# Performance work log

Measured on AMD Instinct MI355X. Metric: run time of the kernel, lower is better.

Reference implementation:

```python
import jax, jax.numpy as jnp
import numpy as np

D_MODEL = 1024
N_HEADS = 16
D_K = D_MODEL // N_HEADS
B, S = 2, 2048
NEG = -1.0e9


def setup_inputs() -> dict:
    key = jax.random.key(0)
    ks = jax.random.split(key, 12)
    sc = 1.0 / np.sqrt(D_MODEL)
    inp = {
        'query': jax.random.normal(ks[0], (B, S, D_MODEL), jnp.float32),
        'key': jax.random.normal(ks[1], (B, S, D_MODEL), jnp.float32),
        'value': jax.random.normal(ks[2], (B, S, D_MODEL), jnp.float32),
        # causal mask, broadcast over batch: 1 = attend, 0 = masked
        'mask': jnp.broadcast_to(jnp.tril(jnp.ones((S, S), jnp.int32)), (B, S, S)),
        'wq': jax.random.normal(ks[3], (D_MODEL, D_MODEL), jnp.float32) * sc,
        'bq': jnp.zeros((D_MODEL,), jnp.float32),
        'wk': jax.random.normal(ks[4], (D_MODEL, D_MODEL), jnp.float32) * sc,
        'bk': jnp.zeros((D_MODEL,), jnp.float32),
        'wv': jax.random.normal(ks[5], (D_MODEL, D_MODEL), jnp.float32) * sc,
        'bv': jnp.zeros((D_MODEL,), jnp.float32),
        'wo': jax.random.normal(ks[6], (D_MODEL, D_MODEL), jnp.float32) * sc,
        'bo': jnp.zeros((D_MODEL,), jnp.float32),
    }
    return inp


def reference(query, key, value, mask, wq, bq, wk, bk, wv, bv, wo, bo):
    b, sq, _ = query.shape
    sk = key.shape[1]
    # linear projections, split into heads: [B, H, S, d_k]
    def proj(x, w, bias, s):
        return (x @ w + bias).reshape(b, s, N_HEADS, D_K).transpose(0, 2, 1, 3)
    Q = proj(query, wq, bq, sq)
    K = proj(key, wk, bk, sk)
    V = proj(value, wv, bv, sk)
    # scaled dot-product attention with full score matrix [B, H, Sq, Sk]
    scores = jnp.einsum('bhqd,bhkd->bhqk', Q, K) / np.sqrt(D_K)
    scores = jnp.where(mask[:, None, :, :] == 0, NEG, scores)
    attn = jax.nn.softmax(scores, axis=-1)
    ctx = jnp.einsum('bhqk,bhkd->bhqd', attn, V)
    ctx = ctx.transpose(0, 2, 1, 3).reshape(b, sq, D_MODEL)
    return ctx @ wo + bo
```

## Files before the change

kernel.cpp:

```cpp
#include <hip/hip_runtime.h>
#include <stdint.h>

#define AS1 __attribute__((address_space(1)))
#define AS3 __attribute__((address_space(3)))

typedef __attribute__((ext_vector_type(8))) __bf16 bf16x8;
typedef __attribute__((ext_vector_type(4))) float f32x4;
typedef __attribute__((ext_vector_type(4))) unsigned int u32x4;
typedef __attribute__((ext_vector_type(2))) unsigned int u32x2;

static __device__ __forceinline__ void gload16(const void* g, void* l) {
    __builtin_amdgcn_global_load_lds((AS1 void*)(uintptr_t)g, (AS3 void*)l, 16, 0, 0);
}

static __device__ __forceinline__ unsigned cvt_pk_bf16(float lo, float hi) {
    unsigned r;
    asm volatile("v_cvt_pk_bf16_f32 %0, %1, %2" : "=v"(r) : "v"(lo), "v"(hi));
    return r;
}
static __device__ __forceinline__ unsigned short f2bf(float f) {
    return (unsigned short)(cvt_pk_bf16(f, 0.f) & 0xffffu);
}

static __device__ __forceinline__ f32x4 mfma16(bf16x8 a, bf16x8 b, f32x4 c) {
    return __builtin_amdgcn_mfma_f32_16x16x32_bf16(a, b, c, 0, 0, 0);
}

static __device__ __forceinline__ float fexp2(float x) {
    return __builtin_amdgcn_exp2f(x);
}

__global__ __launch_bounds__(256) void k_wtrans4(const float* __restrict__ w0,
                                                 const float* __restrict__ w1,
                                                 const float* __restrict__ w2,
                                                 const float* __restrict__ w3,
                                                 unsigned short* __restrict__ o0,
                                                 unsigned short* __restrict__ o1,
                                                 unsigned short* __restrict__ o2,
                                                 unsigned short* __restrict__ o3) {
    const float* W;
    unsigned short* Wt;
    switch (blockIdx.z) {
        case 0: W = w0; Wt = o0; break;
        case 1: W = w1; Wt = o1; break;
        case 2: W = w2; Wt = o2; break;
        default: W = w3; Wt = o3; break;
    }
    __shared__ unsigned short tile[64][72];
    const int tid = threadIdx.x;
    const int k0 = blockIdx.x * 64, n0 = blockIdx.y * 64;
#pragma unroll
    for (int j = 0; j < 4; ++j) {
        int c = j * 256 + tid;
        int kr = c >> 4, c4 = c & 15;
        f32x4 v = *(const f32x4*)(W + (size_t)(k0 + kr) * 1024 + n0 + c4 * 4);
#pragma unroll
        for (int e = 0; e < 4; ++e) tile[c4 * 4 + e][kr] = f2bf(v[e]);
    }
    __syncthreads();
#pragma unroll
    for (int j = 0; j < 2; ++j) {
        int c = j * 256 + tid;
        int nr = c >> 3, kc = c & 7;
        union { unsigned short s[8]; u32x4 v; } t;
#pragma unroll
        for (int e = 0; e < 8; ++e) t.s[e] = tile[nr][kc * 8 + e];
        *(u32x4*)(Wt + (size_t)(n0 + nr) * 1024 + k0 + kc * 8) = t.v;
    }
}

__global__ __launch_bounds__(256) void k_cvt3(const float* __restrict__ q,
                                              const float* __restrict__ k,
                                              const float* __restrict__ v,
                                              unsigned short* __restrict__ oq,
                                              unsigned short* __restrict__ ok,
                                              unsigned short* __restrict__ ov) {
    const float* src; unsigned short* dst;
    switch (blockIdx.z) {
        case 0: src = q; dst = oq; break;
        case 1: src = k; dst = ok; break;
        default: src = v; dst = ov; break;
    }
    const size_t i = ((size_t)blockIdx.x * 256 + threadIdx.x) * 8;
    f32x4 a = *(const f32x4*)(src + i);
    f32x4 b = *(const f32x4*)(src + i + 4);
    u32x4 o;
    o[0] = cvt_pk_bf16(a[0], a[1]);
    o[1] = cvt_pk_bf16(a[2], a[3]);
    o[2] = cvt_pk_bf16(b[0], b[1]);
    o[3] = cvt_pk_bf16(b[2], b[3]);
    *(u32x4*)(dst + i) = o;
}

template <int A_F32, int OUT_F32>
static __device__ __forceinline__ void gemm_body(const void* __restrict__ Ap,
                                                 const unsigned short* __restrict__ Bt,
                                                 const float* __restrict__ bias,
                                                 void* __restrict__ Cp,
                                                 int M, int N, int K, float cscale,
                                                 char* smem) {
    constexpr int ASZ = A_F32 ? 16384 : 8192;
    char* sA = smem;
    char* sB = smem + 2 * ASZ;
    const int tid = threadIdx.x;
    const int wave = tid >> 6, lane = tid & 63, g = lane >> 4, l16 = lane & 15;
    const int wm = wave & 1, wn = wave >> 1;
    const int m0 = blockIdx.x * 64, n0 = blockIdx.y * 128;

    f32x4 acc[2][4];
#pragma unroll
    for (int i = 0; i < 2; ++i)
#pragma unroll
        for (int j = 0; j < 4; ++j) acc[i][j] = (f32x4){0.f, 0.f, 0.f, 0.f};

    auto STAGE = [&](int k0, int buf) {
        if constexpr (A_F32) {
            const float* A = (const float*)Ap;
            char* dst = sA + buf * ASZ;
#pragma unroll
            for (int j = 0; j < 4; ++j) {
                int c = j * 256 + tid;
                int row = c >> 4, w = c & 15, kc = w ^ (row & 15);
                gload16(A + (size_t)(m0 + row) * K + k0 + kc * 4, dst + c * 16);
            }
        } else {
            const unsigned short* A = (const unsigned short*)Ap;
            char* dst = sA + buf * ASZ;
#pragma unroll
            for (int j = 0; j < 2; ++j) {
                int c = j * 256 + tid;
                int row = c >> 3, w = c & 7, kc = w ^ (row & 7);
                gload16(A + (size_t)(m0 + row) * K + k0 + kc * 8, dst + c * 16);
            }
        }
        char* dst = sB + buf * 16384;
#pragma unroll
        for (int j = 0; j < 4; ++j) {
            int c = j * 256 + tid;
            int row = c >> 3, w = c & 7, kc = w ^ (row & 7);
            gload16(Bt + (size_t)(n0 + row) * K + k0 + kc * 8, dst + c * 16);
        }
    };

    const int nkt = K >> 6;
    STAGE(0, 0);
    __syncthreads();
    int cur = 0;
#pragma unroll 1
    for (int kt = 0; kt < nkt; ++kt) {
        if (kt + 1 < nkt) STAGE((kt + 1) << 6, cur ^ 1);
        const char* sAc = sA + cur * ASZ;
        const char* sBc = sB + cur * 16384;
#pragma unroll
        for (int ks = 0; ks < 2; ++ks) {
            bf16x8 af[2];
#pragma unroll
            for (int mi = 0; mi < 2; ++mi) {
                int row = wm * 32 + mi * 16 + l16;
                if constexpr (A_F32) {
                    int c0 = (ks * 8 + g * 2) ^ (row & 15);
                    int c1 = (ks * 8 + g * 2 + 1) ^ (row & 15);
                    f32x4 lo = *(const f32x4*)(sAc + row * 256 + c0 * 16);
                    f32x4 hi = *(const f32x4*)(sAc + row * 256 + c1 * 16);
                    union { unsigned u[4]; bf16x8 v; } cv;
                    cv.u[0] = cvt_pk_bf16(lo[0], lo[1]);
                    cv.u[1] = cvt_pk_bf16(lo[2], lo[3]);
                    cv.u[2] = cvt_pk_bf16(hi[0], hi[1]);
                    cv.u[3] = cvt_pk_bf16(hi[2], hi[3]);
                    af[mi] = cv.v;
                } else {
                    int c = (ks * 4 + g) ^ (row & 7);
                    af[mi] = *(const bf16x8*)(sAc + row * 128 + c * 16);
                }
            }
#pragma unroll
            for (int ni = 0; ni < 4; ++ni) {
                int row = wn * 64 + ni * 16 + l16;
                int c = (ks * 4 + g) ^ (row & 7);
                bf16x8 bfr = *(const bf16x8*)(sBc + row * 128 + c * 16);
#pragma unroll
                for (int mi = 0; mi < 2; ++mi)
                    acc[mi][ni] = mfma16(af[mi], bfr, acc[mi][ni]);
            }
        }
        __syncthreads();
        cur ^= 1;
    }
#pragma unroll
    for (int ni = 0; ni < 4; ++ni) {
        int col = n0 + wn * 64 + ni * 16 + l16;
        float bn = bias[col];
#pragma unroll
        for (int mi = 0; mi < 2; ++mi) {
            int rbase = m0 + wm * 32 + mi * 16 + g * 4;
#pragma unroll
            for (int r = 0; r < 4; ++r) {
                float v = (acc[mi][ni][r] + bn) * cscale;
                if constexpr (OUT_F32)
                    ((float*)Cp)[(size_t)(rbase + r) * N + col] = v;
                else
                    ((unsigned short*)Cp)[(size_t)(rbase + r) * N + col] = f2bf(v);
            }
        }
    }
}

__global__ __launch_bounds__(256) void k_gemm_qkv(
    const unsigned short* __restrict__ Aq, const unsigned short* __restrict__ Ak,
    const unsigned short* __restrict__ Av,
    const unsigned short* __restrict__ Wq, const unsigned short* __restrict__ Wk,
    const unsigned short* __restrict__ Wv,
    const float* __restrict__ bq, const float* __restrict__ bk, const float* __restrict__ bv,
    unsigned short* __restrict__ Q2, unsigned short* __restrict__ K2,
    unsigned short* __restrict__ V2) {
    extern __shared__ __align__(16) char smem[];
    const unsigned short* A; const unsigned short* Bt; const float* bias;
    unsigned short* C; float sc;
    switch (blockIdx.z) {
        case 0:  A = Aq; Bt = Wq; bias = bq; C = Q2; sc = 0.18033688011112042f; break;
        case 1:  A = Ak; Bt = Wk; bias = bk; C = K2; sc = 1.0f; break;
        default: A = Av; Bt = Wv; bias = bv; C = V2; sc = 1.0f; break;
    }
    gemm_body<0, 0>(A, Bt, bias, C, 4096, 1024, 1024, sc, smem);
}

__global__ __launch_bounds__(256) void k_gemm_o(const unsigned short* __restrict__ ctx,
                                                const unsigned short* __restrict__ Wo,
                                                const float* __restrict__ bo,
                                                float* __restrict__ out) {
    extern __shared__ __align__(16) char smem[];
    gemm_body<0, 1>(ctx, Wo, bo, out, 4096, 1024, 1024, 1.0f, smem);
}

__global__ __launch_bounds__(256) void k_vtrans(const unsigned short* __restrict__ V2,
                                                unsigned short* __restrict__ Vt) {
    __shared__ unsigned short tile[64][72];
    const int tid = threadIdx.x;
    const int s0 = blockIdx.x * 64;
    const int bh = blockIdx.y, b = bh >> 4, h = bh & 15;
#pragma unroll
    for (int j = 0; j < 2; ++j) {
        int c = j * 256 + tid;
        int sr = c >> 3, dc = c & 7;
        union { u32x4 v; unsigned short s[8]; } t;
        t.v = *(const u32x4*)(V2 + (size_t)(b * 2048 + s0 + sr) * 1024 + h * 64 + dc * 8);
#pragma unroll
        for (int e = 0; e < 8; ++e) tile[dc * 8 + e][sr] = t.s[e];
    }
    __syncthreads();
#pragma unroll
    for (int j = 0; j < 2; ++j) {
        int c = j * 256 + tid;
        int dr = c >> 3, sc = c & 7;
        union { unsigned short s[8]; u32x4 v; } t;
#pragma unroll
        for (int e = 0; e < 8; ++e) t.s[e] = tile[dr][sc * 8 + e];
        *(u32x4*)(Vt + ((size_t)bh * 64 + dr) * 2048 + s0 + sc * 8) = t.v;
    }
}

__global__ __launch_bounds__(128) void k_attn(const unsigned short* __restrict__ Q2,
                                              const unsigned short* __restrict__ K2,
                                              const unsigned short* __restrict__ Vt,
                                              unsigned short* __restrict__ ctx) {
    __shared__ __align__(16) char sK[8192];
    __shared__ __align__(16) char sV[2][8192];
    __shared__ __align__(16) char sP[2][2][2048];

    const int tid = threadIdx.x, w = tid >> 6, lane = tid & 63;
    const int g = lane >> 4, l16 = lane & 15;
    const int bid = blockIdx.x;
    const int xcd = bid & 7, j = bid >> 3;
    const int bh = xcd * 4 + (j & 3);
    const int t = 31 - (j >> 2);
    const int b = bh >> 4, h = bh & 15;
    const int swzl = (l16 & 7) << 4;

    const int r0 = tid >> 3;
    const int sc0 = (tid & 7) ^ (r0 & 7);
    const unsigned short* ksrc = K2 + (size_t)(b * 2048 + r0) * 1024 + h * 64 + sc0 * 8;
    const unsigned short* vsrc = Vt + ((size_t)bh * 64 + r0) * 2048 + sc0 * 8;
    char* const myp0 = sP[w][0] + l16 * 128;
    char* const myp1 = sP[w][1] + l16 * 128;

    const int wq0 = t * 64 + w * 32;
    const int qg0 = wq0 + l16, qg1 = wq0 + 16 + l16;

    const unsigned short* qp0 = Q2 + (size_t)(b * 2048 + wq0 + l16) * 1024 + h * 64;
    const unsigned short* qp1 = qp0 + 16 * 1024;
    bf16x8 qf00 = *(const bf16x8*)(qp0 + g * 8);
    bf16x8 qf01 = *(const bf16x8*)(qp0 + 32 + g * 8);
    bf16x8 qf10 = *(const bf16x8*)(qp1 + g * 8);
    bf16x8 qf11 = *(const bf16x8*)(qp1 + 32 + g * 8);

    f32x4 accO0[4], accO1[4];
#pragma unroll
    for (int i = 0; i < 4; ++i) {
        accO0[i] = (f32x4){0.f, 0.f, 0.f, 0.f};
        accO1[i] = (f32x4){0.f, 0.f, 0.f, 0.f};
    }
    float m0 = 0.f, m1 = 0.f, lsum0 = 0.f, lsum1 = 0.f;

    const int nkv = t + 1;
#pragma unroll
    for (int rr = 0; rr < 4; ++rr) {
        gload16(ksrc + (size_t)(rr * 16) * 1024, sK + rr * 2048 + tid * 16);
        gload16(vsrc + (size_t)(rr * 16) * 2048, sV[0] + rr * 2048 + tid * 16);
    }
    __syncthreads();

    const unsigned short* kstage = ksrc + 64 * 1024;
    const unsigned short* vstage = vsrc + 64;

#pragma unroll 1
    for (int kt = 0; kt < nkv; ++kt) {
        const int cur = kt & 1;
        const int kv0 = kt * 64;
        float s0[16], s1[16];
        __builtin_amdgcn_s_setprio(1);
#pragma unroll
        for (int blk = 0; blk < 4; ++blk) {
            const int rl = blk * 16 + l16;
            const char* krow = sK + rl * 128;
            bf16x8 kf0 = *(const bf16x8*)(krow + ((g << 4) ^ swzl));
            bf16x8 kf1 = *(const bf16x8*)(krow + (((4 + g) << 4) ^ swzl));
            f32x4 a0 = (f32x4){0.f, 0.f, 0.f, 0.f};
            a0 = mfma16(kf0, qf00, a0);
            a0 = mfma16(kf1, qf01, a0);
            f32x4 a1 = (f32x4){0.f, 0.f, 0.f, 0.f};
            a1 = mfma16(kf0, qf10, a1);
            a1 = mfma16(kf1, qf11, a1);
#pragma unroll
            for (int rr = 0; rr < 4; ++rr) {
                s0[blk * 4 + rr] = a0[rr];
                s1[blk * 4 + rr] = a1[rr];
            }
        }
        __builtin_amdgcn_s_setprio(0);
        __syncthreads();
        if (kt + 1 < nkv) {
#pragma unroll
            for (int rr = 0; rr < 4; ++rr) {
                gload16(kstage + (size_t)(rr * 16) * 1024, sK + rr * 2048 + tid * 16);
                gload16(vstage + (size_t)(rr * 16) * 2048, sV[cur ^ 1] + rr * 2048 + tid * 16);
            }
            kstage += 64 * 1024;
            vstage += 64;
        }
        if (kt == t) {
#pragma unroll
            for (int j2 = 0; j2 < 16; ++j2) {
                int kvg = kv0 + (j2 >> 2) * 16 + g * 4 + (j2 & 3);
                if (kvg > qg0) s0[j2] = -1e9f;
                if (kvg > qg1) s1[j2] = -1e9f;
            }
        }
        float pa0 = 0.f, pa1 = 0.f, pa2 = 0.f, pa3 = 0.f;
        float pb0 = 0.f, pb1 = 0.f, pb2 = 0.f, pb3 = 0.f;
        unsigned pk0[8], pk1[8];
#pragma unroll
        for (int j2 = 0; j2 < 4; ++j2) {
            float a0 = fexp2(s0[4 * j2] - m0);
            float a1 = fexp2(s0[4 * j2 + 1] - m0);
            float a2 = fexp2(s0[4 * j2 + 2] - m0);
            float a3 = fexp2(s0[4 * j2 + 3] - m0);
            pa0 += a0; pa1 += a1; pa2 += a2; pa3 += a3;
            pk0[2 * j2] = cvt_pk_bf16(a0, a1);
            pk0[2 * j2 + 1] = cvt_pk_bf16(a2, a3);
            float b0 = fexp2(s1[4 * j2] - m1);
            float b1 = fexp2(s1[4 * j2 + 1] - m1);
            float b2 = fexp2(s1[4 * j2 + 2] - m1);
            float b3 = fexp2(s1[4 * j2 + 3] - m1);
            pb0 += b0; pb1 += b1; pb2 += b2; pb3 += b3;
            pk1[2 * j2] = cvt_pk_bf16(b0, b1);
            pk1[2 * j2 + 1] = cvt_pk_bf16(b2, b3);
        }
        float ps0 = (pa0 + pa1) + (pa2 + pa3);
        float ps1 = (pb0 + pb1) + (pb2 + pb3);
        if (__any(fmaxf(ps0, ps1) > 16777216.f)) {
            {
                float c1 = fmaxf(fmaxf(s0[0], s0[1]), fmaxf(s0[2], s0[3]));
                c1 = fmaxf(c1, fmaxf(fmaxf(s0[4], s0[5]), fmaxf(s0[6], s0[7])));
                float c2 = fmaxf(fmaxf(s0[8], s0[9]), fmaxf(s0[10], s0[11]));
                c2 = fmaxf(c2, fmaxf(fmaxf(s0[12], s0[13]), fmaxf(s0[14], s0[15])));
                float mx = fmaxf(c1, c2);
                mx = fmaxf(mx, __shfl_xor(mx, 16));
                mx = fmaxf(mx, __shfl_xor(mx, 32));
                float mnew = fmaxf(m0, mx);
                float scl = fexp2(m0 - mnew);
                lsum0 *= scl;
#pragma unroll
                for (int dt = 0; dt < 4; ++dt) accO0[dt] = accO0[dt] * scl;
                m0 = mnew;
                ps0 = 0.f;
#pragma unroll
                for (int j2 = 0; j2 < 8; ++j2) {
                    float p0 = fexp2(s0[2 * j2] - m0);
                    float p1 = fexp2(s0[2 * j2 + 1] - m0);
                    ps0 += p0 + p1;
                    pk0[j2] = cvt_pk_bf16(p0, p1);
                }
            }
            {
                float c1 = fmaxf(fmaxf(s1[0], s1[1]), fmaxf(s1[2], s1[3]));
                c1 = fmaxf(c1, fmaxf(fmaxf(s1[4], s1[5]), fmaxf(s1[6], s1[7])));
                float c2 = fmaxf(fmaxf(s1[8], s1[9]), fmaxf(s1[10], s1[11]));
                c2 = fmaxf(c2, fmaxf(fmaxf(s1[12], s1[13]), fmaxf(s1[14], s1[15])));
                float mx = fmaxf(c1, c2);
                mx = fmaxf(mx, __shfl_xor(mx, 16));
                mx = fmaxf(mx, __shfl_xor(mx, 32));
                float mnew = fmaxf(m1, mx);
                float scl = fexp2(m1 - mnew);
                lsum1 *= scl;
#pragma unroll
                for (int dt = 0; dt < 4; ++dt) accO1[dt] = accO1[dt] * scl;
                m1 = mnew;
                ps1 = 0.f;
#pragma unroll
                for (int j2 = 0; j2 < 8; ++j2) {
                    float p0 = fexp2(s1[2 * j2] - m1);
                    float p1 = fexp2(s1[2 * j2 + 1] - m1);
                    ps1 += p0 + p1;
                    pk1[j2] = cvt_pk_bf16(p0, p1);
                }
            }
        }
        lsum0 += ps0;
        lsum1 += ps1;
#pragma unroll
        for (int blk = 0; blk < 4; ++blk) {
            u32x2 pw0 = {pk0[blk * 2], pk0[blk * 2 + 1]};
            u32x2 pw1 = {pk1[blk * 2], pk1[blk * 2 + 1]};
            *(u32x2*)(myp0 + ((blk * 32 + g * 8) ^ swzl)) = pw0;
            *(u32x2*)(myp1 + ((blk * 32 + g * 8) ^ swzl)) = pw1;
        }
        __builtin_amdgcn_s_setprio(1);
#pragma unroll
        for (int kvh = 0; kvh < 2; ++kvh) {
            bf16x8 pf0 = *(const bf16x8*)(myp0 + ((kvh * 64 + g * 16) ^ swzl));
            bf16x8 pf1 = *(const bf16x8*)(myp1 + ((kvh * 64 + g * 16) ^ swzl));
#pragma unroll
            for (int dt = 0; dt < 4; ++dt) {
                const int rv = dt * 16 + l16;
                bf16x8 vf = *(const bf16x8*)(sV[cur] + rv * 128 + (((kvh * 4 + g) << 4) ^ swzl));
                accO0[dt] = mfma16(vf, pf0, accO0[dt]);
                accO1[dt] = mfma16(vf, pf1, accO1[dt]);
            }
        }
        __builtin_amdgcn_s_setprio(0);
        __syncthreads();
    }
    float v0 = lsum0;
    v0 += __shfl_xor(v0, 16);
    v0 += __shfl_xor(v0, 32);
    float inv0 = 1.f / v0;
    float v1 = lsum1;
    v1 += __shfl_xor(v1, 16);
    v1 += __shfl_xor(v1, 32);
    float inv1 = 1.f / v1;
    unsigned short* cp0 = ctx + (size_t)(b * 2048 + wq0 + l16) * 1024 + h * 64 + g * 4;
    unsigned short* cp1 = cp0 + 16 * 1024;
#pragma unroll
    for (int dt = 0; dt < 4; ++dt) {
        u32x2 o0, o1;
        o0[0] = cvt_pk_bf16(accO0[dt][0] * inv0, accO0[dt][1] * inv0);
        o0[1] = cvt_pk_bf16(accO0[dt][2] * inv0, accO0[dt][3] * inv0);
        o1[0] = cvt_pk_bf16(accO1[dt][0] * inv1, accO1[dt][1] * inv1);
        o1[1] = cvt_pk_bf16(accO1[dt][2] * inv1, accO1[dt][3] * inv1);
        *(u32x2*)(cp0 + dt * 16) = o0;
        *(u32x2*)(cp1 + dt * 16) = o1;
    }
}

extern "C" void kernel_launch(void* const* d_in, const int* in_sizes, int n_in,
                              void* d_out, int out_size, void* d_ws, size_t ws_size,
                              hipStream_t stream) {
    const float* query = (const float*)d_in[0];
    const float* key   = (const float*)d_in[1];
    const float* value = (const float*)d_in[2];
    const float* wq = (const float*)d_in[4];
    const float* bq = (const float*)d_in[5];
    const float* wk = (const float*)d_in[6];
    const float* bk = (const float*)d_in[7];
    const float* wv = (const float*)d_in[8];
    const float* bv = (const float*)d_in[9];
    const float* wo = (const float*)d_in[10];
    const float* bo = (const float*)d_in[11];
    float* out = (float*)d_out;

    char* ws = (char*)d_ws;
    unsigned short* Wtq = (unsigned short*)ws;
    unsigned short* Wtk = Wtq + 1024 * 1024;
    unsigned short* Wtv = Wtk + 1024 * 1024;
    unsigned short* Wto = Wtv + 1024 * 1024;
    unsigned short* Q2  = Wto + 1024 * 1024;
    unsigned short* K2  = Q2 + 4096 * 1024;
    unsigned short* V2  = K2 + 4096 * 1024;
    unsigned short* Aq  = V2 + 4096 * 1024;
    unsigned short* Ak  = Aq + 4096 * 1024;
    unsigned short* Av  = Ak + 4096 * 1024;
    unsigned short* Vt  = Aq;
    unsigned short* ctx = Ak;

    dim3 blk(256);
    k_wtrans4<<<dim3(16, 16, 4), blk, 0, stream>>>(wq, wk, wv, wo, Wtq, Wtk, Wtv, Wto);
    k_cvt3<<<dim3(2048, 1, 3), blk, 0, stream>>>(query, key, value, Aq, Ak, Av);

    k_gemm_qkv<<<dim3(64, 8, 3), blk, 49152, stream>>>(Aq, Ak, Av,
                                                       Wtq, Wtk, Wtv, bq, bk, bv,
                                                       Q2, K2, V2);

    k_vtrans<<<dim3(32, 32), blk, 0, stream>>>(V2, Vt);
    k_attn<<<dim3(1024), dim3(128), 0, stream>>>(Q2, K2, Vt, ctx);

    k_gemm_o<<<dim3(64, 8), blk, 49152, stream>>>(ctx, Wto, bo, out);
}
```

Measured before the change: 116.1 us.

## Pair causal query tiles per block and double-buffer K/V with explicit waitcnt

The attention kernel now launches half as many blocks, and each block handles two query tiles: tile 31-p and tile p. This balances the causal work so every block does the same total number of KV iterations. K and V are double-buffered together in one shared array. The next tile's loads are issued at the top of each iteration with a partial vmcnt wait, so the prefetch overlaps compute instead of being issued after a barrier. The trade-off is fewer blocks, which means less parallelism across CUs, and the manual waitcnt assumes a fixed number of outstanding loads.

```diff
diff --git a/kernel.cpp b/kernel.cpp
--- a/kernel.cpp
+++ b/kernel.cpp
@@ -263,8 +263,7 @@
                                               const unsigned short* __restrict__ K2,
                                               const unsigned short* __restrict__ Vt,
                                               unsigned short* __restrict__ ctx) {
-    __shared__ __align__(16) char sK[8192];
-    __shared__ __align__(16) char sV[2][8192];
+    __shared__ __align__(16) char sKV[2][16384];
     __shared__ __align__(16) char sP[2][2][2048];
 
     const int tid = threadIdx.x, w = tid >> 6, lane = tid & 63;
@@ -272,7 +271,7 @@
     const int bid = blockIdx.x;
     const int xcd = bid & 7, j = bid >> 3;
     const int bh = xcd * 4 + (j & 3);
-    const int t = 31 - (j >> 2);
+    const int p = j >> 2;
     const int b = bh >> 4, h = bh & 15;
     const int swzl = (l16 & 7) << 4;
 
@@ -283,192 +282,197 @@
     char* const myp0 = sP[w][0] + l16 * 128;
     char* const myp1 = sP[w][1] + l16 * 128;
 
-    const int wq0 = t * 64 + w * 32;
-    const int qg0 = wq0 + l16, qg1 = wq0 + 16 + l16;
-
-    const unsigned short* qp0 = Q2 + (size_t)(b * 2048 + wq0 + l16) * 1024 + h * 64;
-    const unsigned short* qp1 = qp0 + 16 * 1024;
-    bf16x8 qf00 = *(const bf16x8*)(qp0 + g * 8);
-    bf16x8 qf01 = *(const bf16x8*)(qp0 + 32 + g * 8);
-    bf16x8 qf10 = *(const bf16x8*)(qp1 + g * 8);
-    bf16x8 qf11 = *(const bf16x8*)(qp1 + 32 + g * 8);
-
-    f32x4 accO0[4], accO1[4];
-#pragma unroll
-    for (int i = 0; i < 4; ++i) {
-        accO0[i] = (f32x4){0.f, 0.f, 0.f, 0.f};
-        accO1[i] = (f32x4){0.f, 0.f, 0.f, 0.f};
-    }
-    float m0 = 0.f, m1 = 0.f, lsum0 = 0.f, lsum1 = 0.f;
-
-    const int nkv = t + 1;
-#pragma unroll
-    for (int rr = 0; rr < 4; ++rr) {
-        gload16(ksrc + (size_t)(rr * 16) * 1024, sK + rr * 2048 + tid * 16);
-        gload16(vsrc + (size_t)(rr * 16) * 2048, sV[0] + rr * 2048 + tid * 16);
-    }
-    __syncthreads();
-
-    const unsigned short* kstage = ksrc + 64 * 1024;
-    const unsigned short* vstage = vsrc + 64;
+    auto STAGE = [&](int kv, int buf) {
+#pragma unroll
+        for (int rr = 0; rr < 4; ++rr) {
+            gload16(ksrc + (size_t)(kv + rr * 16) * 1024, sKV[buf] + rr * 2048 + tid * 16);
+            gload16(vsrc + (size_t)(rr * 16) * 2048 + kv, sKV[buf] + 8192 + rr * 2048 + tid * 16);
+        }
+    };
 
 #pragma unroll 1
-    for (int kt = 0; kt < nkv; ++kt) {
-        const int cur = kt & 1;
-        const int kv0 = kt * 64;
-        float s0[16], s1[16];
-        __builtin_amdgcn_s_setprio(1);
-#pragma unroll
-        for (int blk = 0; blk < 4; ++blk) {
-            const int rl = blk * 16 + l16;
-            const char* krow = sK + rl * 128;
-            bf16x8 kf0 = *(const bf16x8*)(krow + ((g << 4) ^ swzl));
-            bf16x8 kf1 = *(const bf16x8*)(krow + (((4 + g) << 4) ^ swzl));
-            f32x4 a0 = (f32x4){0.f, 0.f, 0.f, 0.f};
-            a0 = mfma16(kf0, qf00, a0);
-            a0 = mfma16(kf1, qf01, a0);
-            f32x4 a1 = (f32x4){0.f, 0.f, 0.f, 0.f};
-            a1 = mfma16(kf0, qf10, a1);
-            a1 = mfma16(kf1, qf11, a1);
-#pragma unroll
-            for (int rr = 0; rr < 4; ++rr) {
-                s0[blk * 4 + rr] = a0[rr];
-                s1[blk * 4 + rr] = a1[rr];
-            }
-        }
-        __builtin_amdgcn_s_setprio(0);
-        __syncthreads();
-        if (kt + 1 < nkv) {
-#pragma unroll
-            for (int rr = 0; rr < 4; ++rr) {
-                gload16(kstage + (size_t)(rr * 16) * 1024, sK + rr * 2048 + tid * 16);
-                gload16(vstage + (size_t)(rr * 16) * 2048, sV[cur ^ 1] + rr * 2048 + tid * 16);
-            }
-            kstage += 64 * 1024;
-            vstage += 64;
-        }
-        if (kt == t) {
-#pragma unroll
-            for (int j2 = 0; j2 < 16; ++j2) {
-                int kvg = kv0 + (j2 >> 2) * 16 + g * 4 + (j2 & 3);
-                if (kvg > qg0) s0[j2] = -1e9f;
-                if (kvg > qg1) s1[j2] = -1e9f;
-            }
-        }
-        float pa0 = 0.f, pa1 = 0.f, pa2 = 0.f, pa3 = 0.f;
-        float pb0 = 0.f, pb1 = 0.f, pb2 = 0.f, pb3 = 0.f;
-        unsigned pk0[8], pk1[8];
-#pragma unroll
-        for (int j2 = 0; j2 < 4; ++j2) {
-            float a0 = fexp2(s0[4 * j2] - m0);
-            float a1 = fexp2(s0[4 * j2 + 1] - m0);
-            float a2 = fexp2(s0[4 * j2 + 2] - m0);
-            float a3 = fexp2(s0[4 * j2 + 3] - m0);
-            pa0 += a0; pa1 += a1; pa2 += a2; pa3 += a3;
-            pk0[2 * j2] = cvt_pk_bf16(a0, a1);
-            pk0[2 * j2 + 1] = cvt_pk_bf16(a2, a3);
-            float b0 = fexp2(s1[4 * j2] - m1);
-            float b1 = fexp2(s1[4 * j2 + 1] - m1);
-            float b2 = fexp2(s1[4 * j2 + 2] - m1);
-            float b3 = fexp2(s1[4 * j2 + 3] - m1);
-            pb0 += b0; pb1 += b1; pb2 += b2; pb3 += b3;
-            pk1[2 * j2] = cvt_pk_bf16(b0, b1);
-            pk1[2 * j2 + 1] = cvt_pk_bf16(b2, b3);
-        }
-        float ps0 = (pa0 + pa1) + (pa2 + pa3);
-        float ps1 = (pb0 + pb1) + (pb2 + pb3);
-        if (__any(fmaxf(ps0, ps1) > 16777216.f)) {
-            {
-                float c1 = fmaxf(fmaxf(s0[0], s0[1]), fmaxf(s0[2], s0[3]));
-                c1 = fmaxf(c1, fmaxf(fmaxf(s0[4], s0[5]), fmaxf(s0[6], s0[7])));
-                float c2 = fmaxf(fmaxf(s0[8], s0[9]), fmaxf(s0[10], s0[11]));
-                c2 = fmaxf(c2, fmaxf(fmaxf(s0[12], s0[13]), fmaxf(s0[14], s0[15])));
-                float mx = fmaxf(c1, c2);
-                mx = fmaxf(mx, __shfl_xor(mx, 16));
-                mx = fmaxf(mx, __shfl_xor(mx, 32));
-                float mnew = fmaxf(m0, mx);
-                float scl = fexp2(m0 - mnew);
-                lsum0 *= scl;
-#pragma unroll
-                for (int dt = 0; dt < 4; ++dt) accO0[dt] = accO0[dt] * scl;
-                m0 = mnew;
-                ps0 = 0.f;
-#pragma unroll
-                for (int j2 = 0; j2 < 8; ++j2) {
-                    float p0 = fexp2(s0[2 * j2] - m0);
-                    float p1 = fexp2(s0[2 * j2 + 1] - m0);
-                    ps0 += p0 + p1;
-                    pk0[j2] = cvt_pk_bf16(p0, p1);
+    for (int t2 = 0; t2 < 2; ++t2) {
+        const int t = t2 ? p : (31 - p);
+        const int wq0 = t * 64 + w * 32;
+        const int qg0 = wq0 + l16, qg1 = wq0 + 16 + l16;
+
+        const unsigned short* qp0 = Q2 + (size_t)(b * 2048 + wq0 + l16) * 1024 + h * 64;
+        const unsigned short* qp1 = qp0 + 16 * 1024;
+        bf16x8 qf00 = *(const bf16x8*)(qp0 + g * 8);
+        bf16x8 qf01 = *(const bf16x8*)(qp0 + 32 + g * 8);
+        bf16x8 qf10 = *(const bf16x8*)(qp1 + g * 8);
+        bf16x8 qf11 = *(const bf16x8*)(qp1 + 32 + g * 8);
+
+        f32x4 accO0[4], accO1[4];
+#pragma unroll
+        for (int i = 0; i < 4; ++i) {
+            accO0[i] = (f32x4){0.f, 0.f, 0.f, 0.f};
+            accO1[i] = (f32x4){0.f, 0.f, 0.f, 0.f};
+        }
+        float m0 = 0.f, m1 = 0.f, lsum0 = 0.f, lsum1 = 0.f;
+
+        const int nkv = t + 1;
+        STAGE(0, 0);
+
+#pragma unroll 1
+        for (int kt = 0; kt < nkv; ++kt) {
+            const int cur = kt & 1;
+            const int kv0 = kt * 64;
+            if (kt + 1 < nkv) {
+                STAGE(kv0 + 64, cur ^ 1);
+                asm volatile("s_waitcnt vmcnt(8)" ::: "memory");
+            } else {
+                asm volatile("s_waitcnt vmcnt(0)" ::: "memory");
+            }
+            __builtin_amdgcn_sched_barrier(0);
+            __builtin_amdgcn_s_barrier();
+            const char* kb = sKV[cur];
+            const char* vb = sKV[cur] + 8192;
+            float s0[16], s1[16];
+            __builtin_amdgcn_s_setprio(1);
+#pragma unroll
+            for (int blk = 0; blk < 4; ++blk) {
+                const int rl = blk * 16 + l16;
+                const char* krow = kb + rl * 128;
+                bf16x8 kf0 = *(const bf16x8*)(krow + ((g << 4) ^ swzl));
+                bf16x8 kf1 = *(const bf16x8*)(krow + (((4 + g) << 4) ^ swzl));
+                f32x4 a0 = (f32x4){0.f, 0.f, 0.f, 0.f};
+                a0 = mfma16(kf0, qf00, a0);
+                a0 = mfma16(kf1, qf01, a0);
+                f32x4 a1 = (f32x4){0.f, 0.f, 0.f, 0.f};
+                a1 = mfma16(kf0, qf10, a1);
+                a1 = mfma16(kf1, qf11, a1);
+#pragma unroll
+                for (int rr = 0; rr < 4; ++rr) {
+                    s0[blk * 4 + rr] = a0[rr];
+                    s1[blk * 4 + rr] = a1[rr];
                 }
             }
-            {
-                float c1 = fmaxf(fmaxf(s1[0], s1[1]), fmaxf(s1[2], s1[3]));
-                c1 = fmaxf(c1, fmaxf(fmaxf(s1[4], s1[5]), fmaxf(s1[6], s1[7])));
-                float c2 = fmaxf(fmaxf(s1[8], s1[9]), fmaxf(s1[10], s1[11]));
-                c2 = fmaxf(c2, fmaxf(fmaxf(s1[12], s1[13]), fmaxf(s1[14], s1[15])));
-                float mx = fmaxf(c1, c2);
-                mx = fmaxf(mx, __shfl_xor(mx, 16));
-                mx = fmaxf(mx, __shfl_xor(mx, 32));
-                float mnew = fmaxf(m1, mx);
-                float scl = fexp2(m1 - mnew);
-                lsum1 *= scl;
-#pragma unroll
-                for (int dt = 0; dt < 4; ++dt) accO1[dt] = accO1[dt] * scl;
-                m1 = mnew;
-                ps1 = 0.f;
-#pragma unroll
-                for (int j2 = 0; j2 < 8; ++j2) {
-                    float p0 = fexp2(s1[2 * j2] - m1);
-                    float p1 = fexp2(s1[2 * j2 + 1] - m1);
-                    ps1 += p0 + p1;
-                    pk1[j2] = cvt_pk_bf16(p0, p1);
+            __builtin_amdgcn_s_setprio(0);
+            if (kt == t) {
+#pragma unroll
+                for (int j2 = 0; j2 < 16; ++j2) {
+                    int kvg = kv0 + (j2 >> 2) * 16 + g * 4 + (j2 & 3);
+                    if (kvg > qg0) s0[j2] = -1e9f;
+                    if (kvg > qg1) s1[j2] = -1e9f;
                 }
             }
-        }
-        lsum0 += ps0;
-        lsum1 += ps1;
-#pragma unroll
-        for (int blk = 0; blk < 4; ++blk) {
-            u32x2 pw0 = {pk0[blk * 2], pk0[blk * 2 + 1]};
-            u32x2 pw1 = {pk1[blk * 2], pk1[blk * 2 + 1]};
-            *(u32x2*)(myp0 + ((blk * 32 + g * 8) ^ swzl)) = pw0;
-            *(u32x2*)(myp1 + ((blk * 32 + g * 8) ^ swzl)) = pw1;
-        }
-        __builtin_amdgcn_s_setprio(1);
-#pragma unroll
-        for (int kvh = 0; kvh < 2; ++kvh) {
-            bf16x8 pf0 = *(const bf16x8*)(myp0 + ((kvh * 64 + g * 16) ^ swzl));
-            bf16x8 pf1 = *(const bf16x8*)(myp1 + ((kvh * 64 + g * 16) ^ swzl));
-#pragma unroll
-            for (int dt = 0; dt < 4; ++dt) {
-                const int rv = dt * 16 + l16;
-                bf16x8 vf = *(const bf16x8*)(sV[cur] + rv * 128 + (((kvh * 4 + g) << 4) ^ swzl));
-                accO0[dt] = mfma16(vf, pf0, accO0[dt]);
-                accO1[dt] = mfma16(vf, pf1, accO1[dt]);
-            }
-        }
-        __builtin_amdgcn_s_setprio(0);
-        __syncthreads();
-    }
-    float v0 = lsum0;
-    v0 += __shfl_xor(v0, 16);
-    v0 += __shfl_xor(v0, 32);
-    float inv0 = 1.f / v0;
-    float v1 = lsum1;
-    v1 += __shfl_xor(v1, 16);
-    v1 += __shfl_xor(v1, 32);
-    float inv1 = 1.f / v1;
-    unsigned short* cp0 = ctx + (size_t)(b * 2048 + wq0 + l16) * 1024 + h * 64 + g * 4;
-    unsigned short* cp1 = cp0 + 16 * 1024;
-#pragma unroll
-    for (int dt = 0; dt < 4; ++dt) {
-        u32x2 o0, o1;
-        o0[0] = cvt_pk_bf16(accO0[dt][0] * inv0, accO0[dt][1] * inv0);
-        o0[1] = cvt_pk_bf16(accO0[dt][2] * inv0, accO0[dt][3] * inv0);
-        o1[0] = cvt_pk_bf16(accO1[dt][0] * inv1, accO1[dt][1] * inv1);
-        o1[1] = cvt_pk_bf16(accO1[dt][2] * inv1, accO1[dt][3] * inv1);
-        *(u32x2*)(cp0 + dt * 16) = o0;
-        *(u32x2*)(cp1 + dt * 16) = o1;
+            float pa0 = 0.f, pa1 = 0.f, pa2 = 0.f, pa3 = 0.f;
+            float pb0 = 0.f, pb1 = 0.f, pb2 = 0.f, pb3 = 0.f;
+            unsigned pk0[8], pk1[8];
+#pragma unroll
+            for (int j2 = 0; j2 < 4; ++j2) {
+                float a0 = fexp2(s0[4 * j2] - m0);
+                float a1 = fexp2(s0[4 * j2 + 1] - m0);
+                float a2 = fexp2(s0[4 * j2 + 2] - m0);
+                float a3 = fexp2(s0[4 * j2 + 3] - m0);
+                pa0 += a0; pa1 += a1; pa2 += a2; pa3 += a3;
+                pk0[2 * j2] = cvt_pk_bf16(a0, a1);
+                pk0[2 * j2 + 1] = cvt_pk_bf16(a2, a3);
+                float b0 = fexp2(s1[4 * j2] - m1);
+                float b1 = fexp2(s1[4 * j2 + 1] - m1);
+                float b2 = fexp2(s1[4 * j2 + 2] - m1);
+                float b3 = fexp2(s1[4 * j2 + 3] - m1);
+                pb0 += b0; pb1 += b1; pb2 += b2; pb3 += b3;
+                pk1[2 * j2] = cvt_pk_bf16(b0, b1);
+                pk1[2 * j2 + 1] = cvt_pk_bf16(b2, b3);
+            }
+            float ps0 = (pa0 + pa1) + (pa2 + pa3);
+            float ps1 = (pb0 + pb1) + (pb2 + pb3);
+            if (__any(fmaxf(ps0, ps1) > 16777216.f)) {
+                {
+                    float c1 = fmaxf(fmaxf(s0[0], s0[1]), fmaxf(s0[2], s0[3]));
+                    c1 = fmaxf(c1, fmaxf(fmaxf(s0[4], s0[5]), fmaxf(s0[6], s0[7])));
+                    float c2 = fmaxf(fmaxf(s0[8], s0[9]), fmaxf(s0[10], s0[11]));
+                    c2 = fmaxf(c2, fmaxf(fmaxf(s0[12], s0[13]), fmaxf(s0[14], s0[15])));
+                    float mx = fmaxf(c1, c2);
+                    mx = fmaxf(mx, __shfl_xor(mx, 16));
+                    mx = fmaxf(mx, __shfl_xor(mx, 32));
+                    float mnew = fmaxf(m0, mx);
+                    float scl = fexp2(m0 - mnew);
+                    lsum0 *= scl;
+#pragma unroll
+                    for (int dt = 0; dt < 4; ++dt) accO0[dt] = accO0[dt] * scl;
+                    m0 = mnew;
+                    ps0 = 0.f;
+#pragma unroll
+                    for (int j2 = 0; j2 < 8; ++j2) {
+                        float p0 = fexp2(s0[2 * j2] - m0);
+                        float p1 = fexp2(s0[2 * j2 + 1] - m0);
+                        ps0 += p0 + p1;
+                        pk0[j2] = cvt_pk_bf16(p0, p1);
+                    }
+                }
+                {
+                    float c1 = fmaxf(fmaxf(s1[0], s1[1]), fmaxf(s1[2], s1[3]));
+                    c1 = fmaxf(c1, fmaxf(fmaxf(s1[4], s1[5]), fmaxf(s1[6], s1[7])));
+                    float c2 = fmaxf(fmaxf(s1[8], s1[9]), fmaxf(s1[10], s1[11]));
+                    c2 = fmaxf(c2, fmaxf(fmaxf(s1[12], s1[13]), fmaxf(s1[14], s1[15])));
+                    float mx = fmaxf(c1, c2);
+                    mx = fmaxf(mx, __shfl_xor(mx, 16));
+                    mx = fmaxf(mx, __shfl_xor(mx, 32));
+                    float mnew = fmaxf(m1, mx);
+                    float scl = fexp2(m1 - mnew);
+                    lsum1 *= scl;
+#pragma unroll
+                    for (int dt = 0; dt < 4; ++dt) accO1[dt] = accO1[dt] * scl;
+                    m1 = mnew;
+                    ps1 = 0.f;
+#pragma unroll
+                    for (int j2 = 0; j2 < 8; ++j2) {
+                        float p0 = fexp2(s1[2 * j2] - m1);
+                        float p1 = fexp2(s1[2 * j2 + 1] - m1);
+                        ps1 += p0 + p1;
+                        pk1[j2] = cvt_pk_bf16(p0, p1);
+                    }
+                }
+            }
+            lsum0 += ps0;
+            lsum1 += ps1;
+#pragma unroll
+            for (int blk = 0; blk < 4; ++blk) {
+                u32x2 pw0 = {pk0[blk * 2], pk0[blk * 2 + 1]};
+                u32x2 pw1 = {pk1[blk * 2], pk1[blk * 2 + 1]};
+                *(u32x2*)(myp0 + ((blk * 32 + g * 8) ^ swzl)) = pw0;
+                *(u32x2*)(myp1 + ((blk * 32 + g * 8) ^ swzl)) = pw1;
+            }
+            __builtin_amdgcn_s_setprio(1);
+#pragma unroll
+            for (int kvh = 0; kvh < 2; ++kvh) {
+                bf16x8 pf0 = *(const bf16x8*)(myp0 + ((kvh * 64 + g * 16) ^ swzl));
+                bf16x8 pf1 = *(const bf16x8*)(myp1 + ((kvh * 64 + g * 16) ^ swzl));
+#pragma unroll
+                for (int dt = 0; dt < 4; ++dt) {
+                    const int rv = dt * 16 + l16;
+                    bf16x8 vf = *(const bf16x8*)(vb + rv * 128 + (((kvh * 4 + g) << 4) ^ swzl));
+                    accO0[dt] = mfma16(vf, pf0, accO0[dt]);
+                    accO1[dt] = mfma16(vf, pf1, accO1[dt]);
+                }
+            }
+            __builtin_amdgcn_s_setprio(0);
+            __builtin_amdgcn_sched_barrier(0);
+            __builtin_amdgcn_s_barrier();
+        }
+        float v0 = lsum0;
+        v0 += __shfl_xor(v0, 16);
+        v0 += __shfl_xor(v0, 32);
+        float inv0 = 1.f / v0;
+        float v1 = lsum1;
+        v1 += __shfl_xor(v1, 16);
+        v1 += __shfl_xor(v1, 32);
+        float inv1 = 1.f / v1;
+        unsigned short* cp0 = ctx + (size_t)(b * 2048 + wq0 + l16) * 1024 + h * 64 + g * 4;
+        unsigned short* cp1 = cp0 + 16 * 1024;
+#pragma unroll
+        for (int dt = 0; dt < 4; ++dt) {
+            u32x2 o0, o1;
+            o0[0] = cvt_pk_bf16(accO0[dt][0] * inv0, accO0[dt][1] * inv0);
+            o0[1] = cvt_pk_bf16(accO0[dt][2] * inv0, accO0[dt][3] * inv0);
+            o1[0] = cvt_pk_bf16(accO1[dt][0] * inv1, accO1[dt][1] * inv1);
+            o1[1] = cvt_pk_bf16(accO1[dt][2] * inv1, accO1[dt][3] * inv1);
+            *(u32x2*)(cp0 + dt * 16) = o0;
+            *(u32x2*)(cp1 + dt * 16) = o1;
+        }
     }
 }
 
@@ -511,7 +515,7 @@
                                                        Q2, K2, V2);
 
     k_vtrans<<<dim3(32, 32), blk, 0, stream>>>(V2, Vt);
-    k_attn<<<dim3(1024), dim3(128), 0, stream>>>(Q2, K2, Vt, ctx);
+    k_attn<<<dim3(512), dim3(128), 0, stream>>>(Q2, K2, Vt, ctx);
 
     k_gemm_o<<<dim3(64, 8), blk, 49152, stream>>>(ctx, Wto, bo, out);
 }
```

New measurement: 126.8 us. 1.09x slower.
